# Kernel optimization log

Hardware: AMD Instinct MI355X
Metric: run time of the kernel (lower is better)

Reference implementation:

```python
import jax, jax.numpy as jnp
import numpy as np

N = 50000      # nodes
E = 800000     # edges (no self loops; added in reference like PyG add_self_loops)
IN = 128       # in_channel
C = 64         # out_channel
K = 64         # cos_num (correlation embedding dim)
H = 1          # heads
NEG_SLOPE = 0.2


def setup_inputs() -> dict:
    key = jax.random.key(0)
    ks = jax.random.split(key, 10)
    x = jax.random.normal(ks[0], (N, IN), dtype=jnp.float32)
    corrs = jax.random.normal(ks[1], (N, K), dtype=jnp.float32)
    # random edges guaranteed to have src != dst (original remove_self_loops)
    src = jax.random.randint(ks[2], (E,), 0, N)
    off = jax.random.randint(ks[3], (E,), 1, N)
    dst = (src + off) % N
    edge_index = jnp.stack([src, dst]).astype(jnp.int32)  # [2, E]
    W = jax.random.normal(ks[4], (IN, H * C), dtype=jnp.float32) / np.sqrt(IN)
    att_i = jax.random.normal(ks[5], (1, H, C), dtype=jnp.float32) * 0.1
    att_j = jax.random.normal(ks[6], (1, H, C), dtype=jnp.float32) * 0.1
    att_em_i = jax.random.normal(ks[7], (1, H, K), dtype=jnp.float32) * 0.1
    att_em_j = jax.random.normal(ks[8], (1, H, K), dtype=jnp.float32) * 0.1
    bias = jnp.zeros((C,), dtype=jnp.float32)
    return {"x": x, "edge_index": edge_index, "corrs": corrs, "W": W,
            "att_i": att_i, "att_j": att_j,
            "att_em_i": att_em_i, "att_em_j": att_em_j, "bias": bias}


def reference(x, edge_index, corrs, W, att_i, att_j, att_em_i, att_em_j, bias):
    # add self loops (original: remove_self_loops then add_self_loops)
    loops = jnp.arange(N, dtype=edge_index.dtype)
    src = jnp.concatenate([edge_index[0], loops])   # [E+N] message sources (x_j)
    dst = jnp.concatenate([edge_index[1], loops])   # [E+N] message targets (x_i)

    g = (x @ W).reshape(N, H, C)                    # linear projection, [N,H,C]
    gj = g[src]                                     # source features per edge [E+N,H,C]
    gi = g[dst]                                     # target features per edge
    ej = corrs[src][:, None, :]                     # [E+N,1,K] broadcast over heads
    ei = corrs[dst][:, None, :]

    # GAT-style score on concatenated key [g || corr]
    alpha = (jnp.sum(gi * att_i, -1) + jnp.sum(ei * att_em_i, -1)
             + jnp.sum(gj * att_j, -1) + jnp.sum(ej * att_em_j, -1))   # [E+N,H]
    alpha = jax.nn.leaky_relu(alpha, NEG_SLOPE)

    # neighbor softmax over incoming edges of each target node (per head)
    amax = jax.ops.segment_max(alpha, dst, num_segments=N)
    ex = jnp.exp(alpha - amax[dst])
    denom = jax.ops.segment_sum(ex, dst, num_segments=N)
    a = ex / (denom[dst] + 1e-16)                   # [E+N,H]

    # scatter-add weighted messages
    out = jax.ops.segment_sum(gj * a[..., None], dst, num_segments=N)  # [N,H,C]
    out = out.mean(axis=1) + bias                    # concat=False -> head mean

    # wrapper: float cast + ReLU
    return jax.nn.relu(out.astype(jnp.float32))
```

## Files before the change

kernel.cpp:

```cpp
#include <hip/hip_runtime.h>
#include <hip/hip_bf16.h>
#include <math.h>

#define IN_DIM 128
#define C_DIM 64
#define BKT_CHUNK 8192
#define BS 64
#define SA_CAP 1440

typedef short bf16x8 __attribute__((ext_vector_type(8)));
typedef float f32x4 __attribute__((ext_vector_type(4)));

static __device__ __forceinline__ unsigned short f2bf(float f) {
    unsigned int u = __float_as_uint(f);
    u += 0x7FFFu + ((u >> 16) & 1u);
    return (unsigned short)(u >> 16);
}
static __device__ __forceinline__ float bf2f(unsigned short h) {
    return __uint_as_float(((unsigned int)h) << 16);
}

__global__ __launch_bounds__(256) void k_gemm_bucket(
    const float* __restrict__ x, const float* __restrict__ W,
    const float* __restrict__ corrs,
    const float* __restrict__ att_i, const float* __restrict__ att_j,
    const float* __restrict__ att_em_i, const float* __restrict__ att_em_j,
    unsigned short* __restrict__ g_bf, float* __restrict__ s_i, float* __restrict__ s_j,
    int N, int GB,
    const int* __restrict__ src, const int* __restrict__ dst,
    int E, int NB, int CAP,
    int* __restrict__ bucket_cnt, unsigned int* __restrict__ staging)
{
    __shared__ __attribute__((aligned(16))) unsigned short WT[2][64][128];
    __shared__ int cnt[1024];
    __shared__ int run[1024];
    __shared__ int cur[1024];

    int tid = threadIdx.x;

    if (blockIdx.x >= GB) {
        for (int i = tid; i < NB; i += 256) cnt[i] = 0;
        __syncthreads();

        int T = E + N;
        int base = (blockIdx.x - GB) * BKT_CHUNK;
#pragma unroll
        for (int k = 0; k < BKT_CHUNK / 256; ++k) {
            int i = base + k * 256 + tid;
            if (i < T) {
                int d = (i < E) ? dst[i] : (i - E);
                atomicAdd(&cnt[d >> 6], 1);
            }
        }
        __syncthreads();
        for (int i = tid; i < NB; i += 256) {
            cur[i] = 0;
            if (cnt[i] > 0) run[i] = atomicAdd(&bucket_cnt[i], cnt[i]);
        }
        __syncthreads();
#pragma unroll
        for (int k = 0; k < BKT_CHUNK / 256; ++k) {
            int i = base + k * 256 + tid;
            if (i < T) {
                int d, s;
                if (i < E) { d = dst[i]; s = src[i]; }
                else       { d = i - E; s = d; }
                int b = d >> 6;
                int ofs = atomicAdd(&cur[b], 1);
                int pos = run[b] + ofs;
                if (pos < CAP)
                    staging[(size_t)b * CAP + pos] =
                        (unsigned)s | ((unsigned)(d & 63) << 16);
            }
        }
        return;
    }

#pragma unroll
    for (int p = 0; p < 8; ++p) {
        int f = p * 1024 + tid * 4;
        f32x4 w4 = *(const f32x4*)(W + f);
        int k  = f >> 6;
        int c0 = f & 63;
#pragma unroll
        for (int i = 0; i < 4; ++i) {
            int c = c0 + i;
            float wv = w4[i];
            unsigned short hi = f2bf(wv);
            unsigned short lo = f2bf(wv - bf2f(hi));
            int ks = k ^ ((c & 7) << 3);
            WT[0][c][ks] = hi;
            WT[1][c][ks] = lo;
        }
    }
    __syncthreads();

    int wv = tid >> 6, lane = tid & 63;
    int mrow = lane & 15;
    int kgrp = lane >> 4;

    float ai[4], aj[4], aei[4], aej[4];
#pragma unroll
    for (int t = 0; t < 4; ++t) {
        ai[t]  = att_i[t * 16 + mrow];
        aj[t]  = att_j[t * 16 + mrow];
        aei[t] = att_em_i[t * 16 + mrow];
        aej[t] = att_em_j[t * 16 + mrow];
    }

    for (int half = 0; half < 2; ++half) {
        int row = blockIdx.x * 128 + half * 64 + wv * 16 + mrow;
        int rowc = min(row, N - 1);

        f32x4 acc[4];
#pragma unroll
        for (int t = 0; t < 4; ++t) { f32x4 z = {0.f, 0.f, 0.f, 0.f}; acc[t] = z; }

        f32x4 xa[4], xb[4];
#pragma unroll
        for (int s = 0; s < 4; ++s) {
            const float* xp = x + (size_t)rowc * IN_DIM + s * 32 + kgrp * 8;
            xa[s] = *(const f32x4*)xp;
            xb[s] = *(const f32x4*)(xp + 4);
        }

#pragma unroll
        for (int s = 0; s < 4; ++s) {
            bf16x8 ah;
#pragma unroll
            for (int i = 0; i < 4; ++i) {
                ah[i]     = (short)f2bf(xa[s][i]);
                ah[4 + i] = (short)f2bf(xb[s][i]);
            }
            int kbase = s * 32 + kgrp * 8;
#pragma unroll
            for (int t = 0; t < 4; ++t) {
                int c  = t * 16 + mrow;
                int ks = kbase ^ ((c & 7) << 3);
                bf16x8 bh = *(const bf16x8*)&WT[0][c][ks];
                bf16x8 bl = *(const bf16x8*)&WT[1][c][ks];
                acc[t] = __builtin_amdgcn_mfma_f32_16x16x32_bf16(ah, bh, acc[t], 0, 0, 0);
                acc[t] = __builtin_amdgcn_mfma_f32_16x16x32_bf16(ah, bl, acc[t], 0, 0, 0);
            }
        }

        int crow_base = blockIdx.x * 128 + half * 64 + wv * 16 + (lane >> 4) * 4;
#pragma unroll
        for (int r = 0; r < 4; ++r) {
            int grow  = crow_base + r;
            int growc = min(grow, N - 1);
            float vi = 0.f, vj = 0.f;
            ushort4 hv;
#pragma unroll
            for (int t = 0; t < 4; ++t) {
                float gv = acc[t][r];
                float cv = corrs[(size_t)growc * 64 + t * 16 + mrow];
                unsigned short h = f2bf(gv);
                if (t == 0) hv.x = h; else if (t == 1) hv.y = h;
                else if (t == 2) hv.z = h; else hv.w = h;
                vi = fmaf(gv, ai[t], fmaf(cv, aei[t], vi));
                vj = fmaf(gv, aj[t], fmaf(cv, aej[t], vj));
            }
            if (grow < N)
                *(ushort4*)(g_bf + (size_t)grow * C_DIM + mrow * 4) = hv;
#pragma unroll
            for (int o = 1; o < 16; o <<= 1) {
                vi += __shfl_xor(vi, o);
                vj += __shfl_xor(vj, o);
            }
            if (mrow == 0 && grow < N) { s_i[grow] = vi; s_j[grow] = vj; }
        }
    }
}

__global__ __launch_bounds__(256) void k_scatter_agg(
    const unsigned int* __restrict__ staging, const int* __restrict__ bucket_cnt,
    int N, int CAP,
    const float* __restrict__ s_i, const float* __restrict__ s_j,
    const unsigned short* __restrict__ g_bf,
    const float* __restrict__ bias, float* __restrict__ out)
{
    __shared__ unsigned int raw[SA_CAP];
    __shared__ unsigned int wrecs[SA_CAP];
    __shared__ int   cnt[BS];
    __shared__ int   off[BS + 1];
    __shared__ int   cur[BS];
    __shared__ float si_l[BS];

    int b = blockIdx.x, tid = threadIdx.x;
    int lo = b * BS;
    int bcnt = min(bucket_cnt[b], CAP);
    const unsigned int* sb = staging + (size_t)b * CAP;

    for (int r = tid; r < bcnt; r += 256) raw[r] = sb[r];
    if (tid < BS) {
        cnt[tid] = 0;
        si_l[tid] = (lo + tid < N) ? s_i[lo + tid] : 0.f;
    }
    __syncthreads();

    for (int r = tid; r < bcnt; r += 256)
        atomicAdd(&cnt[(raw[r] >> 16) & 63], 1);
    __syncthreads();

    if (tid < 64) {
        int s = cnt[tid];
        int incl = s;
#pragma unroll
        for (int o = 1; o < 64; o <<= 1) {
            int u = __shfl_up(incl, o);
            if (tid >= o) incl += u;
        }
        off[tid] = incl - s;
        cur[tid] = incl - s;
        if (tid == 63) off[64] = incl;
    }
    __syncthreads();

    for (int r = tid; r < bcnt; r += 256) {
        unsigned int rec = raw[r];
        int dl   = (rec >> 16) & 63;
        int srcn = rec & 0xFFFFu;
        float a = si_l[dl] + s_j[srcn];
        a = (a > 0.f) ? a : 0.2f * a;
        float w = __expf(a);
        int slot = atomicAdd(&cur[dl], 1);
        wrecs[slot] = ((unsigned)f2bf(w) << 16) | (unsigned)srcn;
    }
    __syncthreads();

    int wave = tid >> 6, lane = tid & 63;
    int grp = lane >> 3;
    int cl  = lane & 7;
    for (int nl = wave; nl < BS; nl += 4) {
        int n = lo + nl;
        if (n >= N) break;
        int start = off[nl];
        int end   = off[nl + 1];

        float a0 = 0.f, a1 = 0.f, a2 = 0.f, a3 = 0.f;
        float a4 = 0.f, a5 = 0.f, a6 = 0.f, a7 = 0.f, den = 0.f;
#pragma unroll 2
        for (int e0 = start; e0 < end; e0 += 8) {
            int e = e0 + grp;
            if (e < end) {
                unsigned int rec = wrecs[e];
                int   srcn = rec & 0xFFFFu;
                float w    = bf2f((unsigned short)(rec >> 16));
                const ushort4* gp = (const ushort4*)(g_bf + (size_t)srcn * C_DIM + (cl << 3));
                ushort4 g0 = gp[0];
                ushort4 g1 = gp[1];
                a0 = fmaf(w, bf2f(g0.x), a0);
                a1 = fmaf(w, bf2f(g0.y), a1);
                a2 = fmaf(w, bf2f(g0.z), a2);
                a3 = fmaf(w, bf2f(g0.w), a3);
                a4 = fmaf(w, bf2f(g1.x), a4);
                a5 = fmaf(w, bf2f(g1.y), a5);
                a6 = fmaf(w, bf2f(g1.z), a6);
                a7 = fmaf(w, bf2f(g1.w), a7);
                den += w;
            }
        }
#pragma unroll
        for (int o = 8; o < 64; o <<= 1) {
            a0  += __shfl_xor(a0, o);
            a1  += __shfl_xor(a1, o);
            a2  += __shfl_xor(a2, o);
            a3  += __shfl_xor(a3, o);
            a4  += __shfl_xor(a4, o);
            a5  += __shfl_xor(a5, o);
            a6  += __shfl_xor(a6, o);
            a7  += __shfl_xor(a7, o);
            den += __shfl_xor(den, o);
        }
        if (grp == 0) {
            float inv = 1.f / (den + 1e-16f);
            float av[8] = {a0, a1, a2, a3, a4, a5, a6, a7};
            float* op = out + (size_t)n * C_DIM;
#pragma unroll
            for (int j = 0; j < 8; ++j) {
                int p  = (cl << 3) + j;
                int ch = ((p & 3) << 4) + (p >> 2);
                op[ch] = fmaxf(fmaf(av[j], inv, bias[ch]), 0.f);
            }
        }
    }
}

extern "C" void kernel_launch(void* const* d_in, const int* in_sizes, int n_in,
                              void* d_out, int out_size, void* d_ws, size_t ws_size,
                              hipStream_t stream)
{
    const float* x        = (const float*)d_in[0];
    const int*   eidx     = (const int*)  d_in[1];
    const float* corrs    = (const float*)d_in[2];
    const float* W        = (const float*)d_in[3];
    const float* att_i    = (const float*)d_in[4];
    const float* att_j    = (const float*)d_in[5];
    const float* att_em_i = (const float*)d_in[6];
    const float* att_em_j = (const float*)d_in[7];
    const float* bias     = (const float*)d_in[8];
    float* out = (float*)d_out;

    int N = in_sizes[0] / IN_DIM;
    int E = in_sizes[1] / 2;
    const int* src = eidx;
    const int* dst = eidx + E;

    int T  = E + N;
    int NB = (N + BS - 1) / BS;
    int CAP = ((T + NB - 1) / NB);
    CAP = CAP + CAP / 4;
    CAP = (CAP + 63) & ~63;
    if (CAP > SA_CAP) CAP = SA_CAP;

    char* ws = (char*)d_ws;
    size_t off = 0;
    auto alloc = [&](size_t bytes) -> void* {
        void* p = ws + off;
        off += (bytes + 255) & ~(size_t)255;
        return p;
    };
    unsigned short* g_bf = (unsigned short*)alloc((size_t)N * C_DIM * sizeof(unsigned short));
    float* s_i       = (float*)alloc((size_t)N * sizeof(float));
    float* s_j       = (float*)alloc((size_t)N * sizeof(float));
    unsigned int* staging = (unsigned int*)alloc((size_t)NB * CAP * sizeof(unsigned int));
    int*   bucket_cnt= (int*)alloc((size_t)1024 * sizeof(int));
    (void)ws_size; (void)n_in; (void)out_size;

    hipMemsetAsync(bucket_cnt, 0, 1024 * sizeof(int), stream);

    int GB = (N + 127) / 128;
    int BB = (T + BKT_CHUNK - 1) / BKT_CHUNK;
    k_gemm_bucket<<<GB + BB, 256, 0, stream>>>(
        x, W, corrs, att_i, att_j, att_em_i, att_em_j, g_bf, s_i, s_j,
        N, GB, src, dst, E, NB, CAP, bucket_cnt, staging);

    k_scatter_agg<<<NB, 256, 0, stream>>>(
        staging, bucket_cnt, N, CAP, s_i, s_j, g_bf, bias, out);
}
```

Baseline: 83.01 us.

## Use coarser 256-node buckets and let four aggregation blocks share each bucket

Bucketing now groups destinations into 256-node buckets, so there are far fewer global bucket counters and each binning block's shared histograms are smaller. The binning chunk size is halved, giving more binning blocks. Each aggregation block handles 64 nodes by scanning the whole 256-node bucket from global memory and filtering for its own quarter. This reads each bucket record four times and drops the shared-memory staging copy in exchange for less contention on the global bucket atomics.

```diff
diff --git a/kernel.cpp b/kernel.cpp
--- a/kernel.cpp
+++ b/kernel.cpp
@@ -4,9 +4,8 @@
 
 #define IN_DIM 128
 #define C_DIM 64
-#define BKT_CHUNK 8192
-#define BS 64
-#define SA_CAP 1440
+#define BKT_CHUNK 4096
+#define WR_CAP 1440
 
 typedef short bf16x8 __attribute__((ext_vector_type(8)));
 typedef float f32x4 __attribute__((ext_vector_type(4)));
@@ -32,14 +31,14 @@
     int* __restrict__ bucket_cnt, unsigned int* __restrict__ staging)
 {
     __shared__ __attribute__((aligned(16))) unsigned short WT[2][64][128];
-    __shared__ int cnt[1024];
-    __shared__ int run[1024];
-    __shared__ int cur[1024];
+    __shared__ int cnt[256];
+    __shared__ int run[256];
+    __shared__ int cur[256];
 
     int tid = threadIdx.x;
 
     if (blockIdx.x >= GB) {
-        for (int i = tid; i < NB; i += 256) cnt[i] = 0;
+        cnt[tid] = 0;
         __syncthreads();
 
         int T = E + N;
@@ -49,14 +48,12 @@
             int i = base + k * 256 + tid;
             if (i < T) {
                 int d = (i < E) ? dst[i] : (i - E);
-                atomicAdd(&cnt[d >> 6], 1);
+                atomicAdd(&cnt[d >> 8], 1);
             }
         }
         __syncthreads();
-        for (int i = tid; i < NB; i += 256) {
-            cur[i] = 0;
-            if (cnt[i] > 0) run[i] = atomicAdd(&bucket_cnt[i], cnt[i]);
-        }
+        if (tid < NB && cnt[tid] > 0) run[tid] = atomicAdd(&bucket_cnt[tid], cnt[tid]);
+        cur[tid] = 0;
         __syncthreads();
 #pragma unroll
         for (int k = 0; k < BKT_CHUNK / 256; ++k) {
@@ -65,12 +62,12 @@
                 int d, s;
                 if (i < E) { d = dst[i]; s = src[i]; }
                 else       { d = i - E; s = d; }
-                int b = d >> 6;
+                int b = d >> 8;
                 int ofs = atomicAdd(&cur[b], 1);
                 int pos = run[b] + ofs;
                 if (pos < CAP)
                     staging[(size_t)b * CAP + pos] =
-                        (unsigned)s | ((unsigned)(d & 63) << 16);
+                        (unsigned)s | ((unsigned)(d & 255) << 16);
             }
         }
         return;
@@ -180,27 +177,29 @@
     const unsigned short* __restrict__ g_bf,
     const float* __restrict__ bias, float* __restrict__ out)
 {
-    __shared__ unsigned int raw[SA_CAP];
-    __shared__ unsigned int wrecs[SA_CAP];
-    __shared__ int   cnt[BS];
-    __shared__ int   off[BS + 1];
-    __shared__ int   cur[BS];
-    __shared__ float si_l[BS];
-
-    int b = blockIdx.x, tid = threadIdx.x;
-    int lo = b * BS;
-    int bcnt = min(bucket_cnt[b], CAP);
-    const unsigned int* sb = staging + (size_t)b * CAP;
-
-    for (int r = tid; r < bcnt; r += 256) raw[r] = sb[r];
-    if (tid < BS) {
+    __shared__ unsigned int wrecs[WR_CAP];
+    __shared__ int   cnt[64];
+    __shared__ int   off[65];
+    __shared__ int   cur[64];
+    __shared__ float si_l[64];
+
+    int blk = blockIdx.x, tid = threadIdx.x;
+    int bb  = blk >> 2;
+    int sub = blk & 3;
+    int lo  = blk * 64;
+    int bcnt = min(bucket_cnt[bb], CAP);
+    const unsigned int* sb = staging + (size_t)bb * CAP;
+
+    if (tid < 64) {
         cnt[tid] = 0;
         si_l[tid] = (lo + tid < N) ? s_i[lo + tid] : 0.f;
     }
     __syncthreads();
 
-    for (int r = tid; r < bcnt; r += 256)
-        atomicAdd(&cnt[(raw[r] >> 16) & 63], 1);
+    for (int r = tid; r < bcnt; r += 256) {
+        int dl = (sb[r] >> 16) & 255;
+        if ((dl >> 6) == sub) atomicAdd(&cnt[dl & 63], 1);
+    }
     __syncthreads();
 
     if (tid < 64) {
@@ -218,25 +217,28 @@
     __syncthreads();
 
     for (int r = tid; r < bcnt; r += 256) {
-        unsigned int rec = raw[r];
-        int dl   = (rec >> 16) & 63;
-        int srcn = rec & 0xFFFFu;
-        float a = si_l[dl] + s_j[srcn];
-        a = (a > 0.f) ? a : 0.2f * a;
-        float w = __expf(a);
-        int slot = atomicAdd(&cur[dl], 1);
-        wrecs[slot] = ((unsigned)f2bf(w) << 16) | (unsigned)srcn;
+        unsigned int rec = sb[r];
+        int dl = (rec >> 16) & 255;
+        if ((dl >> 6) == sub) {
+            int srcn = rec & 0xFFFFu;
+            float a = si_l[dl & 63] + s_j[srcn];
+            a = (a > 0.f) ? a : 0.2f * a;
+            float w = __expf(a);
+            int slot = atomicAdd(&cur[dl & 63], 1);
+            if (slot < WR_CAP)
+                wrecs[slot] = ((unsigned)f2bf(w) << 16) | (unsigned)srcn;
+        }
     }
     __syncthreads();
 
     int wave = tid >> 6, lane = tid & 63;
     int grp = lane >> 3;
     int cl  = lane & 7;
-    for (int nl = wave; nl < BS; nl += 4) {
+    for (int nl = wave; nl < 64; nl += 4) {
         int n = lo + nl;
         if (n >= N) break;
         int start = off[nl];
-        int end   = off[nl + 1];
+        int end   = min(off[nl + 1], WR_CAP);
 
         float a0 = 0.f, a1 = 0.f, a2 = 0.f, a3 = 0.f;
         float a4 = 0.f, a5 = 0.f, a6 = 0.f, a7 = 0.f, den = 0.f;
@@ -308,11 +310,10 @@
     const int* dst = eidx + E;
 
     int T  = E + N;
-    int NB = (N + BS - 1) / BS;
+    int NB = (N + 255) >> 8;
     int CAP = ((T + NB - 1) / NB);
     CAP = CAP + CAP / 4;
     CAP = (CAP + 63) & ~63;
-    if (CAP > SA_CAP) CAP = SA_CAP;
 
     char* ws = (char*)d_ws;
     size_t off = 0;
@@ -325,10 +326,10 @@
     float* s_i       = (float*)alloc((size_t)N * sizeof(float));
     float* s_j       = (float*)alloc((size_t)N * sizeof(float));
     unsigned int* staging = (unsigned int*)alloc((size_t)NB * CAP * sizeof(unsigned int));
-    int*   bucket_cnt= (int*)alloc((size_t)1024 * sizeof(int));
+    int*   bucket_cnt= (int*)alloc(256 * sizeof(int));
     (void)ws_size; (void)n_in; (void)out_size;
 
-    hipMemsetAsync(bucket_cnt, 0, 1024 * sizeof(int), stream);
+    hipMemsetAsync(bucket_cnt, 0, 256 * sizeof(int), stream);
 
     int GB = (N + 127) / 128;
     int BB = (T + BKT_CHUNK - 1) / BKT_CHUNK;
@@ -336,6 +337,7 @@
         x, W, corrs, att_i, att_j, att_em_i, att_em_j, g_bf, s_i, s_j,
         N, GB, src, dst, E, NB, CAP, bucket_cnt, staging);
 
-    k_scatter_agg<<<NB, 256, 0, stream>>>(
+    int NBLK = (N + 63) / 64;
+    k_scatter_agg<<<NBLK, 256, 0, stream>>>(
         staging, bucket_cnt, N, CAP, s_i, s_j, g_bf, bias, out);
 }
```

New measurement: 80.71 us. 1.03x faster.

## Drop W low-part split-bf16 GEMM and overlay shared memory via union

Applied to the files above, without the earlier changes.

Stops splitting W into hi and lo bf16 parts, so the projection GEMM issues half as many MFMAs and needs half the W tile in LDS. The GEMM and bucketing shared arrays are overlaid in a union to shrink the per-block LDS footprint, which may raise occupancy. Bucketing loops are limited to unroll 8, and bounds checks against SA_CAP are added on the wrecs writes and reads. The trade-off is lower GEMM precision, since W is now rounded to bf16 with no correction term.

```diff
diff --git a/kernel.cpp b/kernel.cpp
--- a/kernel.cpp
+++ b/kernel.cpp
@@ -19,6 +19,10 @@
 static __device__ __forceinline__ float bf2f(unsigned short h) {
     return __uint_as_float(((unsigned int)h) << 16);
 }
+
+struct SG { unsigned short WT[64][128]; };
+struct SB { int cnt[1024]; int run[1024]; int cur[1024]; };
+union __attribute__((aligned(16))) SU { SG g; SB b; };
 
 __global__ __launch_bounds__(256) void k_gemm_bucket(
     const float* __restrict__ x, const float* __restrict__ W,
@@ -31,34 +35,31 @@
     int E, int NB, int CAP,
     int* __restrict__ bucket_cnt, unsigned int* __restrict__ staging)
 {
-    __shared__ __attribute__((aligned(16))) unsigned short WT[2][64][128];
-    __shared__ int cnt[1024];
-    __shared__ int run[1024];
-    __shared__ int cur[1024];
-
+    __shared__ SU sm;
     int tid = threadIdx.x;
 
     if (blockIdx.x >= GB) {
-        for (int i = tid; i < NB; i += 256) cnt[i] = 0;
+        for (int i = tid; i < NB; i += 256) sm.b.cnt[i] = 0;
         __syncthreads();
 
         int T = E + N;
         int base = (blockIdx.x - GB) * BKT_CHUNK;
-#pragma unroll
+#pragma unroll 8
         for (int k = 0; k < BKT_CHUNK / 256; ++k) {
             int i = base + k * 256 + tid;
             if (i < T) {
                 int d = (i < E) ? dst[i] : (i - E);
-                atomicAdd(&cnt[d >> 6], 1);
+                atomicAdd(&sm.b.cnt[d >> 6], 1);
             }
         }
         __syncthreads();
         for (int i = tid; i < NB; i += 256) {
-            cur[i] = 0;
-            if (cnt[i] > 0) run[i] = atomicAdd(&bucket_cnt[i], cnt[i]);
+            sm.b.cur[i] = 0;
+            if (sm.b.cnt[i] > 0)
+                sm.b.run[i] = atomicAdd(&bucket_cnt[i], sm.b.cnt[i]);
         }
         __syncthreads();
-#pragma unroll
+#pragma unroll 8
         for (int k = 0; k < BKT_CHUNK / 256; ++k) {
             int i = base + k * 256 + tid;
             if (i < T) {
@@ -66,8 +67,8 @@
                 if (i < E) { d = dst[i]; s = src[i]; }
                 else       { d = i - E; s = d; }
                 int b = d >> 6;
-                int ofs = atomicAdd(&cur[b], 1);
-                int pos = run[b] + ofs;
+                int ofs = atomicAdd(&sm.b.cur[b], 1);
+                int pos = sm.b.run[b] + ofs;
                 if (pos < CAP)
                     staging[(size_t)b * CAP + pos] =
                         (unsigned)s | ((unsigned)(d & 63) << 16);
@@ -85,12 +86,8 @@
 #pragma unroll
         for (int i = 0; i < 4; ++i) {
             int c = c0 + i;
-            float wv = w4[i];
-            unsigned short hi = f2bf(wv);
-            unsigned short lo = f2bf(wv - bf2f(hi));
             int ks = k ^ ((c & 7) << 3);
-            WT[0][c][ks] = hi;
-            WT[1][c][ks] = lo;
+            sm.g.WT[c][ks] = f2bf(w4[i]);
         }
     }
     __syncthreads();
@@ -137,10 +134,8 @@
             for (int t = 0; t < 4; ++t) {
                 int c  = t * 16 + mrow;
                 int ks = kbase ^ ((c & 7) << 3);
-                bf16x8 bh = *(const bf16x8*)&WT[0][c][ks];
-                bf16x8 bl = *(const bf16x8*)&WT[1][c][ks];
+                bf16x8 bh = *(const bf16x8*)&sm.g.WT[c][ks];
                 acc[t] = __builtin_amdgcn_mfma_f32_16x16x32_bf16(ah, bh, acc[t], 0, 0, 0);
-                acc[t] = __builtin_amdgcn_mfma_f32_16x16x32_bf16(ah, bl, acc[t], 0, 0, 0);
             }
         }
 
@@ -225,7 +220,8 @@
         a = (a > 0.f) ? a : 0.2f * a;
         float w = __expf(a);
         int slot = atomicAdd(&cur[dl], 1);
-        wrecs[slot] = ((unsigned)f2bf(w) << 16) | (unsigned)srcn;
+        if (slot < SA_CAP)
+            wrecs[slot] = ((unsigned)f2bf(w) << 16) | (unsigned)srcn;
     }
     __syncthreads();
 
@@ -236,7 +232,7 @@
         int n = lo + nl;
         if (n >= N) break;
         int start = off[nl];
-        int end   = off[nl + 1];
+        int end   = min(off[nl + 1], SA_CAP);
 
         float a0 = 0.f, a1 = 0.f, a2 = 0.f, a3 = 0.f;
         float a4 = 0.f, a5 = 0.f, a6 = 0.f, a7 = 0.f, den = 0.f;
```

Measured after the change: 82.55 us. No clear change (-0.6%).
